# Kernel optimization log

Measured on AMD Instinct MI355X. Metric: run time of the kernel, lower is better.

Reference implementation:

```python
import math
import jax, jax.numpy as jnp
import numpy as np

CHANNELS = 256
NUM_HEADS = 4
GROUPS = 32
EPS = 1e-5


def setup_inputs() -> dict:
    key = jax.random.key(0)
    ks = jax.random.split(key, 7)
    b, c, h, w = 8, CHANNELS, 48, 48
    return {
        "x": jax.random.normal(ks[0], (b, c, h, w), dtype=jnp.float32),
        "gn_w": jax.random.uniform(ks[1], (c,), dtype=jnp.float32),
        "gn_b": jax.random.normal(ks[2], (c,), dtype=jnp.float32) * 0.02,
        "qkv_w": jax.random.normal(ks[3], (3 * c, c), dtype=jnp.float32) * (1.0 / math.sqrt(c)),
        "qkv_b": jax.random.normal(ks[4], (3 * c,), dtype=jnp.float32) * 0.02,
        "proj_w": jax.random.normal(ks[5], (c, c), dtype=jnp.float32) * (1.0 / math.sqrt(c)),
        "proj_b": jax.random.normal(ks[6], (c,), dtype=jnp.float32) * 0.02,
    }


def reference(x, gn_w, gn_b, qkv_w, qkv_b, proj_w, proj_b):
    b, c, h, w = x.shape
    nh = NUM_HEADS
    hd = c // nh
    hw = h * w

    # GroupNorm(32, c): normalize over (c/G, h, w) per group
    xg = x.reshape(b, GROUPS, c // GROUPS, h, w)
    mean = jnp.mean(xg, axis=(2, 3, 4), keepdims=True)
    var = jnp.mean(jnp.square(xg - mean), axis=(2, 3, 4), keepdims=True)
    xn = (xg - mean) * jax.lax.rsqrt(var + EPS)
    xn = xn.reshape(b, c, h, w) * gn_w[None, :, None, None] + gn_b[None, :, None, None]

    # 1x1 conv qkv: per-pixel linear
    qkv = jnp.einsum('bchw,oc->bohw', xn, qkv_w) + qkv_b[None, :, None, None]
    q, k, v = jnp.split(qkv, 3, axis=1)  # each (b, c, h, w)

    # split channels into heads: (b, nh, hd, hw)
    q = q.reshape(b, nh, hd, hw)
    k = k.reshape(b, nh, hd, hw)
    v = v.reshape(b, nh, hd, hw)

    scale = 1.0 / math.sqrt(hd)
    attn = jnp.einsum('bndi,bndj->bnij', q, k) * scale  # (b, nh, hw, hw)
    attn = jax.nn.softmax(attn, axis=-1)
    out = jnp.einsum('bnij,bndj->bndi', attn, v)  # (b, nh, hd, hw)
    out = out.reshape(b, c, h, w)

    out = jnp.einsum('bchw,oc->bohw', out, proj_w) + proj_b[None, :, None, None]
    return x + out
```

## Files before the change

### kernel.cpp

```cpp
#include <hip/hip_runtime.h>
#include <hip/hip_bf16.h>
#include <math.h>

#define NB 8
#define NC 256
#define NHW 2304
#define NH 4
#define HD 64
#define CPG 8
#define GN_EPS 1e-5f

typedef __bf16 bf16;
typedef __bf16 bf16x4 __attribute__((ext_vector_type(4)));
typedef __bf16 bf16x8 __attribute__((ext_vector_type(8)));
typedef float f32x4 __attribute__((ext_vector_type(4)));
typedef float f32x16 __attribute__((ext_vector_type(16)));
typedef int i32x4 __attribute__((ext_vector_type(4)));
typedef unsigned int u32;

#define MFMA16(a, b, c) __builtin_amdgcn_mfma_f32_16x16x32_bf16(a, b, c, 0, 0, 0)
#define MFMA32(a, b, c) __builtin_amdgcn_mfma_f32_32x32x16_bf16(a, b, c, 0, 0, 0)

__device__ __forceinline__ float fexp2(float x) {
  float r;
  asm("v_exp_f32 %0, %1" : "=v"(r) : "v"(x));
  return r;
}

__global__ __launch_bounds__(256) void k_pre(const float* __restrict__ x,
                                             const float* __restrict__ gw,
                                             const float* __restrict__ gb,
                                             const float* __restrict__ qw,
                                             const float* __restrict__ pw,
                                             bf16* __restrict__ xnt,
                                             bf16* __restrict__ wq,
                                             bf16* __restrict__ wp) {
  int t = threadIdx.x;
  if (blockIdx.x < 768) {
    int i = blockIdx.x * 256 + t;
    wq[i] = (bf16)qw[i];
    if (i < NC * NC) wp[i] = (bf16)pw[i];
    return;
  }
  int bid = blockIdx.x - 768;
  int b = bid >> 5;
  int g = bid & 31;
  int c0 = g * CPG;
  const float* xb = x + (b * NC + c0) * NHW;
  float v[CPG][9];
  float s = 0.f, s2 = 0.f;
#pragma unroll
  for (int cc = 0; cc < CPG; ++cc)
#pragma unroll
    for (int k = 0; k < 9; ++k) {
      float val = xb[cc * NHW + k * 256 + t];
      v[cc][k] = val;
      s += val;
      s2 += val * val;
    }
#pragma unroll
  for (int m = 1; m < 64; m <<= 1) {
    s += __shfl_xor(s, m);
    s2 += __shfl_xor(s2, m);
  }
  __shared__ float red[8];
  int wid = t >> 6;
  if ((t & 63) == 0) { red[wid] = s; red[4 + wid] = s2; }
  __syncthreads();
  s = red[0] + red[1] + red[2] + red[3];
  s2 = red[4] + red[5] + red[6] + red[7];
  const float inv_n = 1.0f / (CPG * NHW);
  float mean = s * inv_n;
  float var = s2 * inv_n - mean * mean;
  float rsq = rsqrtf(var + GN_EPS);
  float ka[CPG], kb[CPG];
#pragma unroll
  for (int cc = 0; cc < CPG; ++cc) {
    float wv = gw[c0 + cc];
    ka[cc] = wv * rsq;
    kb[cc] = gb[c0 + cc] - mean * rsq * wv;
  }
  bf16* dst = xnt + b * NHW * NC + c0;
#pragma unroll
  for (int k = 0; k < 9; ++k) {
    bf16x8 o;
#pragma unroll
    for (int cc = 0; cc < CPG; ++cc)
      o[cc] = (bf16)(v[cc][k] * ka[cc] + kb[cc]);
    *reinterpret_cast<bf16x8*>(dst + (k * 256 + t) * NC) = o;
  }
}

__global__ __launch_bounds__(256) void k_qkv(const bf16* __restrict__ xnt,
                                             const bf16* __restrict__ wq,
                                             const float* __restrict__ qkvb,
                                             bf16* __restrict__ qt,
                                             bf16* __restrict__ kt,
                                             bf16* __restrict__ vv) {
  int b = blockIdx.z;
  int i_base = blockIdx.x * 128;
  int o_base = blockIdx.y * 128;
  int t = threadIdx.x;
  int lane = t & 63, wid = t >> 6;
  int wm = (wid >> 1) * 64, wn = (wid & 1) * 64;
  int l15 = lane & 15, g = lane >> 4;
  const bool qk = (o_base < 512);
  const bf16* ab;
  const bf16* bb;
  if (qk) {
    ab = wq + (o_base + wm + l15) * NC + g * 8;
    bb = xnt + ((size_t)b * NHW + i_base + wn + l15) * NC + g * 8;
  } else {
    ab = xnt + ((size_t)b * NHW + i_base + wm + l15) * NC + g * 8;
    bb = wq + (o_base + wn + l15) * NC + g * 8;
  }
  f32x4 acc[4][4] = {};
#pragma unroll 2
  for (int kc = 0; kc < 8; ++kc) {
    bf16x8 af[4], bf[4];
#pragma unroll
    for (int mf = 0; mf < 4; ++mf)
      af[mf] = *reinterpret_cast<const bf16x8*>(ab + mf * 16 * NC + kc * 32);
#pragma unroll
    for (int nf = 0; nf < 4; ++nf)
      bf[nf] = *reinterpret_cast<const bf16x8*>(bb + nf * 16 * NC + kc * 32);
#pragma unroll
    for (int mf = 0; mf < 4; ++mf)
#pragma unroll
      for (int nf = 0; nf < 4; ++nf)
        acc[mf][nf] = MFMA16(af[mf], bf[nf], acc[mf][nf]);
  }
  if (qk) {
    const float qscale = 0.125f * 1.4426950408889634f;
#pragma unroll
    for (int mf = 0; mf < 4; ++mf) {
      int o0 = o_base + wm + mf * 16 + g * 4;
      f32x4 b4 = *reinterpret_cast<const f32x4*>(qkvb + o0);
      bool isQ = (o0 < 256);
      float sc = isQ ? qscale : 1.0f;
      int oo = isQ ? o0 : o0 - 256;
      bf16* base = (isQ ? qt : kt) +
                   ((size_t)(b * NH + (oo >> 6)) * NHW) * HD + (oo & 63);
#pragma unroll
      for (int nf = 0; nf < 4; ++nf) {
        int i = i_base + wn + nf * 16 + l15;
        bf16x4 w;
#pragma unroll
        for (int r = 0; r < 4; ++r)
          w[r] = (bf16)((acc[mf][nf][r] + b4[r]) * sc);
        *reinterpret_cast<bf16x4*>(base + (size_t)i * HD) = w;
      }
    }
  } else {
#pragma unroll
    for (int nf = 0; nf < 4; ++nf) {
      int og = o_base + wn + nf * 16 + l15;
      float bias = qkvb[og];
      int o2 = og - 512;
      bf16* dp = vv + ((size_t)(b * NH + (o2 >> 6)) * HD + (o2 & 63)) * NHW +
                 i_base + wm + g * 4;
#pragma unroll
      for (int mf = 0; mf < 4; ++mf) {
        bf16x4 w;
#pragma unroll
        for (int r = 0; r < 4; ++r) w[r] = (bf16)(acc[mf][nf][r] + bias);
        *reinterpret_cast<bf16x4*>(dp + mf * 16) = w;
      }
    }
  }
}

__global__ __launch_bounds__(256, 3) void k_attn(const bf16* __restrict__ qt,
                                                 const bf16* __restrict__ kt,
                                                 const bf16* __restrict__ vv,
                                                 bf16* __restrict__ att) {
  __shared__ union SM {
    struct { bf16 k[2][4096]; bf16 v[2][4096]; } kv;
    float m[2][64][33];
  } smem;

  const int tid = threadIdx.x;
  const int wid = tid >> 6, lane = tid & 63;
  const int l31 = lane & 31, g2 = lane >> 5;
  const int ig = wid & 1, jsub = wid >> 1;

  const int bid = blockIdx.x;
  const int wg = (bid & 7) * 144 + (bid >> 3);
  const int bh = wg / 36, it = wg % 36;
  const int b = bh >> 2, n = bh & 3;
  const int i0w = it * 64 + ig * 32;

  const bf16* qb = qt + (size_t)bh * NHW * HD;
  const bf16* kb = kt + (size_t)bh * NHW * HD;
  const bf16* vb = vv + (size_t)bh * HD * NHW;

  const int r0 = tid >> 3, cs = tid & 7;
  const bf16* kg0 = kb + r0 * HD + cs * 8;
  const bf16* kg1 = kb + (r0 + 32) * HD + cs * 8;
  const bf16* vg0 = vb + (size_t)r0 * NHW + cs * 8;
  const bf16* vg1 = vb + (size_t)(r0 + 32) * NHW + cs * 8;
#define EOFF(c, row) ((c) * 512 + ((((row) + (c)) & 63) << 3))
  const int lw0 = EOFF(cs, r0);
  const int lw1 = EOFF(cs, r0 + 32);

  int ksw[4];
#pragma unroll
  for (int kk = 0; kk < 4; ++kk) ksw[kk] = EOFF(2 * kk + g2, jsub * 32 + l31);
  int vsw0[2], vsw1[2];
#pragma unroll
  for (int J = 0; J < 2; ++J) {
    int c = jsub * 4 + J * 2 + g2;
    vsw0[J] = EOFF(c, l31);
    vsw1[J] = EOFF(c, l31 + 32);
  }
#undef EOFF

  bf16x8 q[4];
#pragma unroll
  for (int kk = 0; kk < 4; ++kk)
    q[kk] = *reinterpret_cast<const bf16x8*>(qb + (i0w + l31) * HD + kk * 16 + g2 * 8);

  f32x16 acc0 = {}, acc1 = {};
  f32x16 sO;
  float l_r = 0.f;

  {
    bf16x8 a = *reinterpret_cast<const bf16x8*>(kg0);
    bf16x8 c = *reinterpret_cast<const bf16x8*>(kg1);
    *reinterpret_cast<bf16x8*>(&smem.kv.k[0][lw0]) = a;
    *reinterpret_cast<bf16x8*>(&smem.kv.k[0][lw1]) = c;
  }
  asm volatile("s_waitcnt lgkmcnt(0)" ::: "memory");
  __builtin_amdgcn_s_barrier();

  {
    bf16x8 kr0 = *reinterpret_cast<const bf16x8*>(kg0 + 64 * HD);
    bf16x8 kr1 = *reinterpret_cast<const bf16x8*>(kg1 + 64 * HD);
    bf16x8 vr0 = *reinterpret_cast<const bf16x8*>(vg0);
    bf16x8 vr1 = *reinterpret_cast<const bf16x8*>(vg1);
    const bf16* kc = smem.kv.k[0];
    f32x16 s = {};
    __builtin_amdgcn_s_setprio(1);
#pragma unroll
    for (int kk = 0; kk < 4; ++kk) {
      bf16x8 kf = *reinterpret_cast<const bf16x8*>(kc + ksw[kk]);
      s = MFMA32(kf, q[kk], s);
    }
    __builtin_amdgcn_s_setprio(0);
    *reinterpret_cast<bf16x8*>(&smem.kv.k[1][lw0]) = kr0;
    *reinterpret_cast<bf16x8*>(&smem.kv.k[1][lw1]) = kr1;
    *reinterpret_cast<bf16x8*>(&smem.kv.v[0][lw0]) = vr0;
    *reinterpret_cast<bf16x8*>(&smem.kv.v[0][lw1]) = vr1;
    asm volatile("s_waitcnt lgkmcnt(0)" ::: "memory");
    __builtin_amdgcn_s_barrier();
    sO = s;
  }

  for (int t = 1; t < 36; ++t) {
    bf16x8 kr0, kr1;
    if (t < 35) {
      kr0 = *reinterpret_cast<const bf16x8*>(kg0 + (t + 1) * (64 * HD));
      kr1 = *reinterpret_cast<const bf16x8*>(kg1 + (t + 1) * (64 * HD));
    }
    bf16x8 vr0 = *reinterpret_cast<const bf16x8*>(vg0 + t * 64);
    bf16x8 vr1 = *reinterpret_cast<const bf16x8*>(vg1 + t * 64);

    const bf16* kc = smem.kv.k[t & 1];
    const bf16* vcp = smem.kv.v[(t - 1) & 1];

    bf16x8 kf[4], vf0[2], vf1[2];
#pragma unroll
    for (int kk = 0; kk < 4; ++kk)
      kf[kk] = *reinterpret_cast<const bf16x8*>(kc + ksw[kk]);
#pragma unroll
    for (int J = 0; J < 2; ++J) {
      vf0[J] = *reinterpret_cast<const bf16x8*>(vcp + vsw0[J]);
      vf1[J] = *reinterpret_cast<const bf16x8*>(vcp + vsw1[J]);
    }

    u32 P[8];
    float la = 0.f, lb = 0.f;
#pragma unroll
    for (int m = 0; m < 8; ++m) {
      float e0 = fexp2(sO[2 * m]);
      float e1 = fexp2(sO[2 * m + 1]);
      la += e0;
      lb += e1;
      u32 pk;
      asm("v_cvt_pk_bf16_f32 %0, %1, %2" : "=v"(pk) : "v"(e0), "v"(e1));
      P[m] = pk;
    }
    l_r += la + lb;
    bf16x8 pf[2];
#pragma unroll
    for (int J = 0; J < 2; ++J) {
      u32 w0 = P[4 * J], w2 = P[4 * J + 2];
      asm("v_permlane32_swap_b32 %0, %1" : "+v"(w0), "+v"(w2));
      u32 w1 = P[4 * J + 1], w3 = P[4 * J + 3];
      asm("v_permlane32_swap_b32 %0, %1" : "+v"(w1), "+v"(w3));
      i32x4 wv;
      wv[0] = (int)w0; wv[1] = (int)w1; wv[2] = (int)w2; wv[3] = (int)w3;
      pf[J] = __builtin_bit_cast(bf16x8, wv);
    }

    f32x16 s = {};
    __builtin_amdgcn_s_setprio(1);
#pragma unroll
    for (int kk = 0; kk < 4; ++kk) s = MFMA32(kf[kk], q[kk], s);
#pragma unroll
    for (int J = 0; J < 2; ++J) {
      acc0 = MFMA32(vf0[J], pf[J], acc0);
      acc1 = MFMA32(vf1[J], pf[J], acc1);
    }
    __builtin_amdgcn_s_setprio(0);

    if (t < 35) {
      *reinterpret_cast<bf16x8*>(&smem.kv.k[(t + 1) & 1][lw0]) = kr0;
      *reinterpret_cast<bf16x8*>(&smem.kv.k[(t + 1) & 1][lw1]) = kr1;
    }
    *reinterpret_cast<bf16x8*>(&smem.kv.v[t & 1][lw0]) = vr0;
    *reinterpret_cast<bf16x8*>(&smem.kv.v[t & 1][lw1]) = vr1;
    asm volatile("s_waitcnt lgkmcnt(0)" ::: "memory");
    __builtin_amdgcn_s_barrier();
    sO = s;
  }

  {
    u32 P[8];
    float la = 0.f, lb = 0.f;
#pragma unroll
    for (int m = 0; m < 8; ++m) {
      float e0 = fexp2(sO[2 * m]);
      float e1 = fexp2(sO[2 * m + 1]);
      la += e0;
      lb += e1;
      u32 pk;
      asm("v_cvt_pk_bf16_f32 %0, %1, %2" : "=v"(pk) : "v"(e0), "v"(e1));
      P[m] = pk;
    }
    l_r += la + lb;
    const bf16* vcp = smem.kv.v[1];
#pragma unroll
    for (int J = 0; J < 2; ++J) {
      u32 w0 = P[4 * J], w2 = P[4 * J + 2];
      asm("v_permlane32_swap_b32 %0, %1" : "+v"(w0), "+v"(w2));
      u32 w1 = P[4 * J + 1], w3 = P[4 * J + 3];
      asm("v_permlane32_swap_b32 %0, %1" : "+v"(w1), "+v"(w3));
      i32x4 wv;
      wv[0] = (int)w0; wv[1] = (int)w1; wv[2] = (int)w2; wv[3] = (int)w3;
      bf16x8 pf = __builtin_bit_cast(bf16x8, wv);
      bf16x8 v0 = *reinterpret_cast<const bf16x8*>(vcp + vsw0[J]);
      bf16x8 v1 = *reinterpret_cast<const bf16x8*>(vcp + vsw1[J]);
      acc0 = MFMA32(v0, pf, acc0);
      acc1 = MFMA32(v1, pf, acc1);
    }
  }

  __builtin_amdgcn_s_barrier();
  if (jsub == 1) {
    float* mb = smem.m[ig][lane];
#pragma unroll
    for (int e = 0; e < 16; ++e) { mb[e] = acc0[e]; mb[16 + e] = acc1[e]; }
    mb[32] = l_r;
  }
  __syncthreads();
  if (jsub == 0) {
    const float* mb = smem.m[ig][lane];
#pragma unroll
    for (int e = 0; e < 16; ++e) { acc0[e] += mb[e]; acc1[e] += mb[16 + e]; }
    l_r += mb[32];
    l_r += __shfl_xor(l_r, 32);
    const float inv = 1.0f / l_r;
    bf16* ob = att + ((size_t)(b * NHW) + i0w + l31) * NC + n * HD;
#pragma unroll
    for (int rq = 0; rq < 4; ++rq) {
      bf16x4 o0, o1;
#pragma unroll
      for (int c = 0; c < 4; ++c) {
        o0[c] = (bf16)(acc0[rq * 4 + c] * inv);
        o1[c] = (bf16)(acc1[rq * 4 + c] * inv);
      }
      *reinterpret_cast<bf16x4*>(ob + 8 * rq + 4 * g2) = o0;
      *reinterpret_cast<bf16x4*>(ob + 32 + 8 * rq + 4 * g2) = o1;
    }
  }
}

__global__ __launch_bounds__(256) void k_proj(const bf16* __restrict__ att,
                                              const bf16* __restrict__ wp,
                                              const float* __restrict__ pb,
                                              const float* __restrict__ x,
                                              float* __restrict__ out) {
  int b = blockIdx.z;
  int i_base = blockIdx.x * 128;
  int o_base = blockIdx.y * 128;
  int t = threadIdx.x;
  int lane = t & 63, wid = t >> 6;
  int wm = (wid >> 1) * 64, wn = (wid & 1) * 64;
  int l15 = lane & 15, g = lane >> 4;
  const bf16* ab = wp + (o_base + wm + l15) * NC + g * 8;
  const bf16* bb = att + (b * NHW + i_base + wn + l15) * NC + g * 8;
  f32x4 acc[4][4] = {};
#pragma unroll 2
  for (int kc = 0; kc < 8; ++kc) {
    bf16x8 af[4], bf[4];
#pragma unroll
    for (int mf = 0; mf < 4; ++mf)
      af[mf] = *reinterpret_cast<const bf16x8*>(ab + mf * 16 * NC + kc * 32);
#pragma unroll
    for (int nf = 0; nf < 4; ++nf)
      bf[nf] = *reinterpret_cast<const bf16x8*>(bb + nf * 16 * NC + kc * 32);
#pragma unroll
    for (int mf = 0; mf < 4; ++mf)
#pragma unroll
      for (int nf = 0; nf < 4; ++nf)
        acc[mf][nf] = MFMA16(af[mf], bf[nf], acc[mf][nf]);
  }
  int orow0 = o_base + wm + g * 4;
#pragma unroll
  for (int mf = 0; mf < 4; ++mf)
#pragma unroll
    for (int r = 0; r < 4; ++r) {
      int o = orow0 + mf * 16 + r;
      float bias = pb[o];
      const float* xr = x + (b * NC + o) * NHW + i_base + wn;
      float* orow = out + (b * NC + o) * NHW + i_base + wn;
#pragma unroll
      for (int nf = 0; nf < 4; ++nf) {
        int i = nf * 16 + l15;
        orow[i] = acc[mf][nf][r] + bias + xr[i];
      }
    }
}

extern "C" void kernel_launch(void* const* d_in, const int* in_sizes, int n_in,
                              void* d_out, int out_size, void* d_ws, size_t ws_size,
                              hipStream_t stream) {
  const float* x    = (const float*)d_in[0];
  const float* gnw  = (const float*)d_in[1];
  const float* gnb  = (const float*)d_in[2];
  const float* qkvw = (const float*)d_in[3];
  const float* qkvb = (const float*)d_in[4];
  const float* pw   = (const float*)d_in[5];
  const float* pb   = (const float*)d_in[6];
  float* out = (float*)d_out;

  bf16* ws = (bf16*)d_ws;
  const size_t NE = (size_t)NB * NHW * NC;
  bf16* xnt = ws;
  bf16* qt  = ws + NE;
  bf16* kt  = ws + 2 * NE;
  bf16* vv  = ws + 3 * NE;
  bf16* att = ws + 4 * NE;
  bf16* wqb = ws + 5 * NE;
  bf16* wpb = wqb + 768 * 256;

  k_pre<<<1024, 256, 0, stream>>>(x, gnw, gnb, qkvw, pw, xnt, wqb, wpb);
  k_qkv<<<dim3(18, 6, NB), 256, 0, stream>>>(xnt, wqb, qkvb, qt, kt, vv);
  k_attn<<<1152, 256, 0, stream>>>(qt, kt, vv, att);
  k_proj<<<dim3(18, 2, NB), 256, 0, stream>>>(att, wpb, pb, x, out);
}
```

Measured before the change: 149.5 us.

## Enlarge attention workgroup to 128 query rows with 8 waves sharing K/V tiles

The attention kernel now runs 512-thread workgroups, each covering 128 query rows with four query-row waves and two key-split waves, instead of 64 rows with 256 threads. Each K/V tile staged in shared memory is reused by twice as many queries, which halves global K/V loads per query and gives each thread one load instead of two. The final cross-wave merge is split into two passes through a smaller shared buffer so the shared-memory footprint stays the same. The cost is extra barriers in the epilogue, larger workgroups, and a grid of 576 blocks, which may load-balance less evenly across CUs.

```diff
diff --git a/kernel.cpp b/kernel.cpp
--- a/kernel.cpp
+++ b/kernel.cpp
@@ -170,38 +170,35 @@
   }
 }
 
-__global__ __launch_bounds__(256, 3) void k_attn(const bf16* __restrict__ qt,
+__global__ __launch_bounds__(512, 4) void k_attn(const bf16* __restrict__ qt,
                                                  const bf16* __restrict__ kt,
                                                  const bf16* __restrict__ vv,
                                                  bf16* __restrict__ att) {
   __shared__ union SM {
     struct { bf16 k[2][4096]; bf16 v[2][4096]; } kv;
-    float m[2][64][33];
+    float m[4][64][17];
   } smem;
 
   const int tid = threadIdx.x;
   const int wid = tid >> 6, lane = tid & 63;
   const int l31 = lane & 31, g2 = lane >> 5;
-  const int ig = wid & 1, jsub = wid >> 1;
+  const int ig = wid & 3, jsub = wid >> 2;
 
   const int bid = blockIdx.x;
-  const int wg = (bid & 7) * 144 + (bid >> 3);
-  const int bh = wg / 36, it = wg % 36;
+  const int wg = (bid & 7) * 72 + (bid >> 3);
+  const int bh = wg / 18, it = wg % 18;
   const int b = bh >> 2, n = bh & 3;
-  const int i0w = it * 64 + ig * 32;
+  const int i0w = it * 128 + ig * 32;
 
   const bf16* qb = qt + (size_t)bh * NHW * HD;
   const bf16* kb = kt + (size_t)bh * NHW * HD;
   const bf16* vb = vv + (size_t)bh * HD * NHW;
 
   const int r0 = tid >> 3, cs = tid & 7;
-  const bf16* kg0 = kb + r0 * HD + cs * 8;
-  const bf16* kg1 = kb + (r0 + 32) * HD + cs * 8;
-  const bf16* vg0 = vb + (size_t)r0 * NHW + cs * 8;
-  const bf16* vg1 = vb + (size_t)(r0 + 32) * NHW + cs * 8;
+  const bf16* kg = kb + r0 * HD + cs * 8;
+  const bf16* vg = vb + (size_t)r0 * NHW + cs * 8;
 #define EOFF(c, row) ((c) * 512 + ((((row) + (c)) & 63) << 3))
-  const int lw0 = EOFF(cs, r0);
-  const int lw1 = EOFF(cs, r0 + 32);
+  const int lw = EOFF(cs, r0);
 
   int ksw[4];
 #pragma unroll
@@ -225,19 +222,15 @@
   float l_r = 0.f;
 
   {
-    bf16x8 a = *reinterpret_cast<const bf16x8*>(kg0);
-    bf16x8 c = *reinterpret_cast<const bf16x8*>(kg1);
-    *reinterpret_cast<bf16x8*>(&smem.kv.k[0][lw0]) = a;
-    *reinterpret_cast<bf16x8*>(&smem.kv.k[0][lw1]) = c;
+    bf16x8 a = *reinterpret_cast<const bf16x8*>(kg);
+    *reinterpret_cast<bf16x8*>(&smem.kv.k[0][lw]) = a;
   }
   asm volatile("s_waitcnt lgkmcnt(0)" ::: "memory");
   __builtin_amdgcn_s_barrier();
 
   {
-    bf16x8 kr0 = *reinterpret_cast<const bf16x8*>(kg0 + 64 * HD);
-    bf16x8 kr1 = *reinterpret_cast<const bf16x8*>(kg1 + 64 * HD);
-    bf16x8 vr0 = *reinterpret_cast<const bf16x8*>(vg0);
-    bf16x8 vr1 = *reinterpret_cast<const bf16x8*>(vg1);
+    bf16x8 kr = *reinterpret_cast<const bf16x8*>(kg + 64 * HD);
+    bf16x8 vr = *reinterpret_cast<const bf16x8*>(vg);
     const bf16* kc = smem.kv.k[0];
     f32x16 s = {};
     __builtin_amdgcn_s_setprio(1);
@@ -247,23 +240,18 @@
       s = MFMA32(kf, q[kk], s);
     }
     __builtin_amdgcn_s_setprio(0);
-    *reinterpret_cast<bf16x8*>(&smem.kv.k[1][lw0]) = kr0;
-    *reinterpret_cast<bf16x8*>(&smem.kv.k[1][lw1]) = kr1;
-    *reinterpret_cast<bf16x8*>(&smem.kv.v[0][lw0]) = vr0;
-    *reinterpret_cast<bf16x8*>(&smem.kv.v[0][lw1]) = vr1;
+    *reinterpret_cast<bf16x8*>(&smem.kv.k[1][lw]) = kr;
+    *reinterpret_cast<bf16x8*>(&smem.kv.v[0][lw]) = vr;
     asm volatile("s_waitcnt lgkmcnt(0)" ::: "memory");
     __builtin_amdgcn_s_barrier();
     sO = s;
   }
 
   for (int t = 1; t < 36; ++t) {
-    bf16x8 kr0, kr1;
-    if (t < 35) {
-      kr0 = *reinterpret_cast<const bf16x8*>(kg0 + (t + 1) * (64 * HD));
-      kr1 = *reinterpret_cast<const bf16x8*>(kg1 + (t + 1) * (64 * HD));
-    }
-    bf16x8 vr0 = *reinterpret_cast<const bf16x8*>(vg0 + t * 64);
-    bf16x8 vr1 = *reinterpret_cast<const bf16x8*>(vg1 + t * 64);
+    bf16x8 kr, vr;
+    if (t < 35)
+      kr = *reinterpret_cast<const bf16x8*>(kg + (t + 1) * (64 * HD));
+    vr = *reinterpret_cast<const bf16x8*>(vg + t * 64);
 
     const bf16* kc = smem.kv.k[t & 1];
     const bf16* vcp = smem.kv.v[(t - 1) & 1];
@@ -314,12 +302,9 @@
     }
     __builtin_amdgcn_s_setprio(0);
 
-    if (t < 35) {
-      *reinterpret_cast<bf16x8*>(&smem.kv.k[(t + 1) & 1][lw0]) = kr0;
-      *reinterpret_cast<bf16x8*>(&smem.kv.k[(t + 1) & 1][lw1]) = kr1;
-    }
-    *reinterpret_cast<bf16x8*>(&smem.kv.v[t & 1][lw0]) = vr0;
-    *reinterpret_cast<bf16x8*>(&smem.kv.v[t & 1][lw1]) = vr1;
+    if (t < 35)
+      *reinterpret_cast<bf16x8*>(&smem.kv.k[(t + 1) & 1][lw]) = kr;
+    *reinterpret_cast<bf16x8*>(&smem.kv.v[t & 1][lw]) = vr;
     asm volatile("s_waitcnt lgkmcnt(0)" ::: "memory");
     __builtin_amdgcn_s_barrier();
     sO = s;
@@ -355,20 +340,32 @@
       acc1 = MFMA32(v1, pf, acc1);
     }
   }
-
   __builtin_amdgcn_s_barrier();
+
   if (jsub == 1) {
     float* mb = smem.m[ig][lane];
 #pragma unroll
-    for (int e = 0; e < 16; ++e) { mb[e] = acc0[e]; mb[16 + e] = acc1[e]; }
-    mb[32] = l_r;
+    for (int e = 0; e < 16; ++e) mb[e] = acc0[e];
+    mb[16] = l_r;
   }
   __syncthreads();
   if (jsub == 0) {
     const float* mb = smem.m[ig][lane];
 #pragma unroll
-    for (int e = 0; e < 16; ++e) { acc0[e] += mb[e]; acc1[e] += mb[16 + e]; }
-    l_r += mb[32];
+    for (int e = 0; e < 16; ++e) acc0[e] += mb[e];
+    l_r += mb[16];
+  }
+  __syncthreads();
+  if (jsub == 1) {
+    float* mb = smem.m[ig][lane];
+#pragma unroll
+    for (int e = 0; e < 16; ++e) mb[e] = acc1[e];
+  }
+  __syncthreads();
+  if (jsub == 0) {
+    const float* mb = smem.m[ig][lane];
+#pragma unroll
+    for (int e = 0; e < 16; ++e) acc1[e] += mb[e];
     l_r += __shfl_xor(l_r, 32);
     const float inv = 1.0f / l_r;
     bf16* ob = att + ((size_t)(b * NHW) + i0w + l31) * NC + n * HD;
@@ -457,6 +454,6 @@
 
   k_pre<<<1024, 256, 0, stream>>>(x, gnw, gnb, qkvw, pw, xnt, wqb, wpb);
   k_qkv<<<dim3(18, 6, NB), 256, 0, stream>>>(xnt, wqb, qkvb, qt, kt, vv);
-  k_attn<<<1152, 256, 0, stream>>>(qt, kt, vv, att);
+  k_attn<<<576, 512, 0, stream>>>(qt, kt, vv, att);
   k_proj<<<dim3(18, 2, NB), 256, 0, stream>>>(att, wpb, pb, x, out);
 }
```

Measured after the change: 163.4 us. +9.3%, slower.
